# Performance work log

Measured on AMD Instinct MI355X. Metric: run time of the kernel, lower is better.

The kernel has to match this reference:

```python
import jax, jax.numpy as jnp
import numpy as np


def setup_inputs() -> dict:
    key = jax.random.key(0)
    k1, k2, k3 = jax.random.split(key, 3)
    N, C, H, W, K = 4, 128, 40, 30, 64
    return {
        "x": jax.random.normal(k1, (N, C, H, W), dtype=jnp.float32),
        "conv_w": jax.random.normal(k2, (K, C), dtype=jnp.float32) * 0.1,  # 1x1 conv weight [K,C,1,1] squeezed
        "centroids": jax.random.uniform(k3, (K, C), dtype=jnp.float32),
        "patch_size": 5,
        "stride": 1,
    }


def reference(x, conv_w, centroids, patch_size, stride):
    N, C, H, W = x.shape
    K = centroids.shape[0]
    # descriptor-wise L2 normalization (torch F.normalize semantics, eps=1e-12)
    norm = jnp.sqrt(jnp.sum(x * x, axis=1, keepdims=True))
    xn = x / jnp.maximum(norm, 1e-12)
    # 1x1 conv (no bias) + softmax over clusters -> soft assignment [N,K,H,W]
    logits = jnp.einsum('nchw,kc->nkhw', xn, conv_w)
    sa = jax.nn.softmax(logits, axis=1)
    # residuals [N,K,C,H,W]: (x - c_k) * a_k, then flatten K,C
    res = (xn[:, None, :, :, :] - centroids[None, :, :, None, None]) * sa[:, :, None, :, :]
    res = res.reshape(N, K * C, H, W)
    # 2D integral image with top-left zero padding -> [N,KC,H+1,W+1]
    I = jnp.cumsum(jnp.cumsum(res, axis=-1), axis=-2)
    I = jnp.pad(I, ((0, 0), (0, 0), (1, 0), (1, 0)))
    # box-filter via integral-image differencing (equivalent to the grouped
    # dilated 2x2 conv with weights [[+1,-1],[-1,+1]], stride=s, dilation=p)
    p, s = int(patch_size), int(stride)
    out = (I[:, :, p::s, p::s] - I[:, :, p::s, :-p:s]
           - I[:, :, :-p:s, p::s] + I[:, :, :-p:s, :-p:s])
    return out / (p * p)
```

## Files before the change

kernel.cpp:

```cpp
#include <hip/hip_runtime.h>

#define C_ 128
#define K_ 64
#define H_ 40
#define W_ 30
#define N_ 4
#define HW_ 1200
#define P_ 5
#define OH_ 36
#define OW_ 26
#define OHW_ 936

template<int CTRL>
__device__ __forceinline__ float dpp0f(float v) {
  return __int_as_float(__builtin_amdgcn_update_dpp(
      0, __float_as_int(v), CTRL, 0xF, 0xF, true));
}
__device__ __forceinline__ float swz_x16(float v) {
  return __int_as_float(__builtin_amdgcn_ds_swizzle(__float_as_int(v), 0x401F));
}

__global__ __launch_bounds__(256) void k1_prep(
    const float* __restrict__ x, const float* __restrict__ cw,
    float* __restrict__ xn, float* __restrict__ sa)
{
  __shared__ float xs[C_][32];
  __shared__ float wt[C_][K_];
  __shared__ float part[8][32];
  __shared__ float ls[K_][32];
  __shared__ float rnorm_s[32];
  __shared__ float rsum_s[32];

  const int tid  = threadIdx.x;
  const int pix0 = blockIdx.x << 5;

  for (int e = tid; e < C_*K_; e += 256) {
    const int c = e >> 6, kk = e & 63;
    wt[c][kk] = cw[kk*C_ + c];
  }
  for (int e = tid; e < C_*32; e += 256) {
    const int c = e >> 5, pl = e & 31;
    const int pix = pix0 + pl;
    const int n = pix / HW_, rem = pix - n*HW_;
    xs[c][pl] = x[(size_t)(n*C_ + c)*HW_ + rem];
  }
  __syncthreads();
  {
    const int pl = tid & 31, cq = tid >> 5;
    float s = 0.f;
    #pragma unroll
    for (int cc = 0; cc < 16; ++cc) {
      const float v = xs[cq*16 + cc][pl];
      s = fmaf(v, v, s);
    }
    part[cq][pl] = s;
  }
  __syncthreads();
  if (tid < 32) {
    float s = 0.f;
    #pragma unroll
    for (int qq = 0; qq < 8; ++qq) s += part[qq][tid];
    rnorm_s[tid] = 1.f / fmaxf(sqrtf(s), 1e-12f);
  }
  __syncthreads();
  {
    const int pl = tid & 31, kq = tid >> 5;
    float acc[8];
    #pragma unroll
    for (int qq = 0; qq < 8; ++qq) acc[qq] = 0.f;
    for (int c = 0; c < C_; ++c) {
      const float xv = xs[c][pl];
      const float4 w0 = *(const float4*)&wt[c][kq*8];
      const float4 w1 = *(const float4*)&wt[c][kq*8 + 4];
      acc[0] = fmaf(xv, w0.x, acc[0]);
      acc[1] = fmaf(xv, w0.y, acc[1]);
      acc[2] = fmaf(xv, w0.z, acc[2]);
      acc[3] = fmaf(xv, w0.w, acc[3]);
      acc[4] = fmaf(xv, w1.x, acc[4]);
      acc[5] = fmaf(xv, w1.y, acc[5]);
      acc[6] = fmaf(xv, w1.z, acc[6]);
      acc[7] = fmaf(xv, w1.w, acc[7]);
    }
    const float rn = rnorm_s[pl];
    #pragma unroll
    for (int qq = 0; qq < 8; ++qq) ls[kq*8 + qq][pl] = acc[qq] * rn;
  }
  __syncthreads();
  if (tid < 32) {
    const int pl = tid;
    float m = -1e30f;
    for (int kk = 0; kk < K_; ++kk) m = fmaxf(m, ls[kk][pl]);
    float s = 0.f;
    for (int kk = 0; kk < K_; ++kk) {
      const float e = expf(ls[kk][pl] - m);
      ls[kk][pl] = e;
      s += e;
    }
    rsum_s[pl] = 1.f / s;
  }
  __syncthreads();
  for (int e = tid; e < K_*32; e += 256) {
    const int kk = e >> 5, pl = e & 31;
    const int pix = pix0 + pl;
    const int n = pix / HW_, rem = pix - n*HW_;
    sa[(size_t)(n*K_ + kk)*HW_ + rem] = ls[kk][pl] * rsum_s[pl];
  }
  for (int e = tid; e < C_*32; e += 256) {
    const int c = e >> 5, pl = e & 31;
    const int pix = pix0 + pl;
    const int n = pix / HW_, rem = pix - n*HW_;
    xn[(size_t)(n*C_ + c)*HW_ + rem] = xs[c][pl] * rnorm_s[pl];
  }
}

__global__ __launch_bounds__(256, 6) void k2_box(
    const float* __restrict__ xn, const float* __restrict__ sa,
    const float* __restrict__ cent, float* __restrict__ out)
{
  const int tid = threadIdx.x;
  const int w   = tid & 31;
  const int wc  = (w < W_) ? w : (W_ - 1);
  const int c   = (blockIdx.x << 3) + (tid >> 5);
  const int k   = blockIdx.y;
  const int nh  = blockIdx.z;
  const int n   = nh >> 1;
  const int r0  = (nh & 1) * 18;

  const float cv = cent[k*C_ + c];
  const float* __restrict__ xp = xn + (size_t)(n*C_ + c)*HW_ + (size_t)r0*W_ + wc;
  const float* __restrict__ sp = sa + (size_t)(n*K_ + k)*HW_ + (size_t)r0*W_ + wc;

  float q[22];
  #pragma unroll
  for (int h = 0; h < 22; ++h) {
    q[h] = (xp[h*W_] - cv) * sp[h*W_];
  }

  float vq = q[0] + q[1] + q[2] + q[3] + q[4];
  float* __restrict__ op = out + (size_t)((n*K_ + k)*C_ + c)*OHW_
                               + (size_t)r0*OW_ + w;

  #pragma unroll
  for (int i = 0; i < 18; ++i) {
    const float sw = swz_x16(vq);
    float hs = vq;
    hs += dpp0f<0x101>(vq) + dpp0f<0x11F>(sw);
    hs += dpp0f<0x102>(vq) + dpp0f<0x11E>(sw);
    hs += dpp0f<0x103>(vq) + dpp0f<0x11D>(sw);
    hs += dpp0f<0x104>(vq) + dpp0f<0x11C>(sw);
    if (w < OW_) op[i*OW_] = hs * (1.f / (P_*P_));
    if (i < 17) vq += q[i + P_] - q[i];
  }
}

extern "C" void kernel_launch(void* const* d_in, const int* in_sizes, int n_in,
                              void* d_out, int out_size, void* d_ws, size_t ws_size,
                              hipStream_t stream) {
  const float* x  = (const float*)d_in[0];
  const float* cw = (const float*)d_in[1];
  const float* ce = (const float*)d_in[2];

  float* xn = (float*)d_ws;
  float* sa = xn + (size_t)N_*C_*HW_;
  float* out = (float*)d_out;

  k1_prep<<<dim3(150), dim3(256), 0, stream>>>(x, cw, xn, sa);
  k2_box<<<dim3(C_/8, K_, N_*2), dim3(256), 0, stream>>>(xn, sa, ce, out);
}
```

Before: 46.04 us.

## Split prep kernel into norm, logits, and softmax kernels

Replaces the single shared-memory prep kernel with three kernels: per-pixel L2 norm plus normalized output, a logits GEMV spread over 8 cluster groups per pixel block, and a softmax across 4 waves with a shared-memory reduction. The goal is more parallelism in the prep stage, which previously ran in only 150 blocks with serial single-wave softmax and transpose-staged weights. In exchange it adds two more kernel launches, a logits round trip through global memory, and reads x twice.

```diff
diff --git a/kernel.cpp b/kernel.cpp
--- a/kernel.cpp
+++ b/kernel.cpp
@@ -20,97 +20,112 @@
   return __int_as_float(__builtin_amdgcn_ds_swizzle(__float_as_int(v), 0x401F));
 }
 
-__global__ __launch_bounds__(256) void k1_prep(
+__global__ __launch_bounds__(64) void k1a_norm(
+    const float* __restrict__ x, float* __restrict__ xn,
+    float* __restrict__ rnorm)
+{
+  const int apix = (blockIdx.x << 6) + threadIdx.x;
+  const int n   = apix / HW_;
+  const int rem = apix - n*HW_;
+  const float* __restrict__ xp = x + (size_t)n*C_*HW_ + rem;
+
+  float s0 = 0.f, s1 = 0.f, s2 = 0.f, s3 = 0.f;
+  #pragma unroll 8
+  for (int c = 0; c < C_; c += 4) {
+    const float v0 = xp[(c+0)*HW_];
+    const float v1 = xp[(c+1)*HW_];
+    const float v2 = xp[(c+2)*HW_];
+    const float v3 = xp[(c+3)*HW_];
+    s0 = fmaf(v0, v0, s0); s1 = fmaf(v1, v1, s1);
+    s2 = fmaf(v2, v2, s2); s3 = fmaf(v3, v3, s3);
+  }
+  const float rn = 1.f / fmaxf(sqrtf((s0 + s1) + (s2 + s3)), 1e-12f);
+  rnorm[apix] = rn;
+
+  float* __restrict__ xo = xn + (size_t)n*C_*HW_ + rem;
+  #pragma unroll 8
+  for (int c = 0; c < C_; ++c) xo[c*HW_] = xp[c*HW_] * rn;
+}
+
+__global__ __launch_bounds__(64) void k1b_logits(
     const float* __restrict__ x, const float* __restrict__ cw,
-    float* __restrict__ xn, float* __restrict__ sa)
+    const float* __restrict__ rnorm, float* __restrict__ logits)
 {
-  __shared__ float xs[C_][32];
-  __shared__ float wt[C_][K_];
-  __shared__ float part[8][32];
-  __shared__ float ls[K_][32];
-  __shared__ float rnorm_s[32];
-  __shared__ float rsum_s[32];
+  const int apix = (blockIdx.x << 6) + threadIdx.x;
+  const int kq   = blockIdx.y;
+  const int n   = apix / HW_;
+  const int rem = apix - n*HW_;
+  const float* __restrict__ xp = x + (size_t)n*C_*HW_ + rem;
 
-  const int tid  = threadIdx.x;
-  const int pix0 = blockIdx.x << 5;
+  float acc[8];
+  #pragma unroll
+  for (int j = 0; j < 8; ++j) acc[j] = 0.f;
 
-  for (int e = tid; e < C_*K_; e += 256) {
-    const int c = e >> 6, kk = e & 63;
-    wt[c][kk] = cw[kk*C_ + c];
+  for (int c0 = 0; c0 < C_; c0 += 16) {
+    float xv[16];
+    #pragma unroll
+    for (int j = 0; j < 16; ++j) xv[j] = xp[(c0 + j)*HW_];
+    #pragma unroll
+    for (int kk = 0; kk < 8; ++kk) {
+      const float* __restrict__ wr = cw + (kq*8 + kk)*C_ + c0;
+      const float4 w0 = *(const float4*)(wr + 0);
+      const float4 w1 = *(const float4*)(wr + 4);
+      const float4 w2 = *(const float4*)(wr + 8);
+      const float4 w3 = *(const float4*)(wr + 12);
+      float a = acc[kk];
+      a = fmaf(w0.x, xv[0],  a); a = fmaf(w0.y, xv[1],  a);
+      a = fmaf(w0.z, xv[2],  a); a = fmaf(w0.w, xv[3],  a);
+      a = fmaf(w1.x, xv[4],  a); a = fmaf(w1.y, xv[5],  a);
+      a = fmaf(w1.z, xv[6],  a); a = fmaf(w1.w, xv[7],  a);
+      a = fmaf(w2.x, xv[8],  a); a = fmaf(w2.y, xv[9],  a);
+      a = fmaf(w2.z, xv[10], a); a = fmaf(w2.w, xv[11], a);
+      a = fmaf(w3.x, xv[12], a); a = fmaf(w3.y, xv[13], a);
+      a = fmaf(w3.z, xv[14], a); a = fmaf(w3.w, xv[15], a);
+      acc[kk] = a;
+    }
   }
-  for (int e = tid; e < C_*32; e += 256) {
-    const int c = e >> 5, pl = e & 31;
-    const int pix = pix0 + pl;
-    const int n = pix / HW_, rem = pix - n*HW_;
-    xs[c][pl] = x[(size_t)(n*C_ + c)*HW_ + rem];
-  }
+  const float rn = rnorm[apix];
+  float* __restrict__ lp = logits + (size_t)(n*K_ + kq*8)*HW_ + rem;
+  #pragma unroll
+  for (int kk = 0; kk < 8; ++kk) lp[kk*HW_] = acc[kk] * rn;
+}
+
+__global__ __launch_bounds__(256) void k1c_softmax(
+    const float* __restrict__ logits, float* __restrict__ sa)
+{
+  __shared__ float red[8][64];
+
+  const int lane = threadIdx.x & 63;
+  const int wv   = threadIdx.x >> 6;
+  const int apix = (blockIdx.x << 6) + lane;
+  const int n   = apix / HW_;
+  const int rem = apix - n*HW_;
+  const float* __restrict__ lp = logits + (size_t)(n*K_ + wv*16)*HW_ + rem;
+
+  float v[16];
+  #pragma unroll
+  for (int j = 0; j < 16; ++j) v[j] = lp[j*HW_];
+
+  float mx = v[0];
+  #pragma unroll
+  for (int j = 1; j < 16; ++j) mx = fmaxf(mx, v[j]);
+  red[wv][lane] = mx;
   __syncthreads();
-  {
-    const int pl = tid & 31, cq = tid >> 5;
-    float s = 0.f;
-    #pragma unroll
-    for (int cc = 0; cc < 16; ++cc) {
-      const float v = xs[cq*16 + cc][pl];
-      s = fmaf(v, v, s);
-    }
-    part[cq][pl] = s;
-  }
+  mx = fmaxf(fmaxf(red[0][lane], red[1][lane]),
+             fmaxf(red[2][lane], red[3][lane]));
+
+  float e[16];
+  float sum = 0.f;
+  #pragma unroll
+  for (int j = 0; j < 16; ++j) { e[j] = expf(v[j] - mx); sum += e[j]; }
+  red[4 + wv][lane] = sum;
   __syncthreads();
-  if (tid < 32) {
-    float s = 0.f;
-    #pragma unroll
-    for (int qq = 0; qq < 8; ++qq) s += part[qq][tid];
-    rnorm_s[tid] = 1.f / fmaxf(sqrtf(s), 1e-12f);
-  }
-  __syncthreads();
-  {
-    const int pl = tid & 31, kq = tid >> 5;
-    float acc[8];
-    #pragma unroll
-    for (int qq = 0; qq < 8; ++qq) acc[qq] = 0.f;
-    for (int c = 0; c < C_; ++c) {
-      const float xv = xs[c][pl];
-      const float4 w0 = *(const float4*)&wt[c][kq*8];
-      const float4 w1 = *(const float4*)&wt[c][kq*8 + 4];
-      acc[0] = fmaf(xv, w0.x, acc[0]);
-      acc[1] = fmaf(xv, w0.y, acc[1]);
-      acc[2] = fmaf(xv, w0.z, acc[2]);
-      acc[3] = fmaf(xv, w0.w, acc[3]);
-      acc[4] = fmaf(xv, w1.x, acc[4]);
-      acc[5] = fmaf(xv, w1.y, acc[5]);
-      acc[6] = fmaf(xv, w1.z, acc[6]);
-      acc[7] = fmaf(xv, w1.w, acc[7]);
-    }
-    const float rn = rnorm_s[pl];
-    #pragma unroll
-    for (int qq = 0; qq < 8; ++qq) ls[kq*8 + qq][pl] = acc[qq] * rn;
-  }
-  __syncthreads();
-  if (tid < 32) {
-    const int pl = tid;
-    float m = -1e30f;
-    for (int kk = 0; kk < K_; ++kk) m = fmaxf(m, ls[kk][pl]);
-    float s = 0.f;
-    for (int kk = 0; kk < K_; ++kk) {
-      const float e = expf(ls[kk][pl] - m);
-      ls[kk][pl] = e;
-      s += e;
-    }
-    rsum_s[pl] = 1.f / s;
-  }
-  __syncthreads();
-  for (int e = tid; e < K_*32; e += 256) {
-    const int kk = e >> 5, pl = e & 31;
-    const int pix = pix0 + pl;
-    const int n = pix / HW_, rem = pix - n*HW_;
-    sa[(size_t)(n*K_ + kk)*HW_ + rem] = ls[kk][pl] * rsum_s[pl];
-  }
-  for (int e = tid; e < C_*32; e += 256) {
-    const int c = e >> 5, pl = e & 31;
-    const int pix = pix0 + pl;
-    const int n = pix / HW_, rem = pix - n*HW_;
-    xn[(size_t)(n*C_ + c)*HW_ + rem] = xs[c][pl] * rnorm_s[pl];
-  }
+  const float rs = 1.f / (((red[4][lane] + red[5][lane]) +
+                           (red[6][lane] + red[7][lane])));
+
+  float* __restrict__ sp = sa + (size_t)(n*K_ + wv*16)*HW_ + rem;
+  #pragma unroll
+  for (int j = 0; j < 16; ++j) sp[j*HW_] = e[j] * rs;
 }
 
 __global__ __launch_bounds__(256, 6) void k2_box(
@@ -160,10 +175,14 @@
   const float* cw = (const float*)d_in[1];
   const float* ce = (const float*)d_in[2];
 
-  float* xn = (float*)d_ws;
-  float* sa = xn + (size_t)N_*C_*HW_;
+  float* xn     = (float*)d_ws;
+  float* sa     = xn + (size_t)N_*C_*HW_;
+  float* logits = sa + (size_t)N_*K_*HW_;
+  float* rnorm  = logits + (size_t)N_*K_*HW_;
   float* out = (float*)d_out;
 
-  k1_prep<<<dim3(150), dim3(256), 0, stream>>>(x, cw, xn, sa);
-  k2_box<<<dim3(C_/8, K_, N_*2), dim3(256), 0, stream>>>(xn, sa, ce, out);
+  k1a_norm   <<<dim3(75),     dim3(64),  0, stream>>>(x, xn, rnorm);
+  k1b_logits <<<dim3(75, 8),  dim3(64),  0, stream>>>(x, cw, rnorm, logits);
+  k1c_softmax<<<dim3(75),     dim3(256), 0, stream>>>(logits, sa);
+  k2_box     <<<dim3(C_/8, K_, N_*2), dim3(256), 0, stream>>>(xn, sa, ce, out);
 }
```

Measured after the change: 64.41 us. 39.9% more time.

## Restructure prep kernel: 16-pixel tiles, vectorized IO, parallel softmax reductions

Applied to the files above, without the earlier changes.

The prep kernel now handles 16 pixels per block, which doubles the grid to 300 blocks. It drops the transposed weight copy in shared memory and reads conv weights straight from global memory as float4. Loads and stores of x, xn and sa are vectorized, and the softmax max and sum are split across all threads through a partial-reduction array instead of 32 serial threads. This targets the serial tail and the low block count in the prep stage, but that stage is likely a small share of total time next to the box kernel, which writes a large output.

```diff
diff --git a/kernel.cpp b/kernel.cpp
--- a/kernel.cpp
+++ b/kernel.cpp
@@ -10,6 +10,7 @@
 #define OH_ 36
 #define OW_ 26
 #define OHW_ 936
+#define PIX_ 16
 
 template<int CTRL>
 __device__ __forceinline__ float dpp0f(float v) {
@@ -20,96 +21,144 @@
   return __int_as_float(__builtin_amdgcn_ds_swizzle(__float_as_int(v), 0x401F));
 }
 
-__global__ __launch_bounds__(256) void k1_prep(
+__global__ __launch_bounds__(256) void k1_fused(
     const float* __restrict__ x, const float* __restrict__ cw,
     float* __restrict__ xn, float* __restrict__ sa)
 {
-  __shared__ float xs[C_][32];
-  __shared__ float wt[C_][K_];
-  __shared__ float part[8][32];
-  __shared__ float ls[K_][32];
-  __shared__ float rnorm_s[32];
-  __shared__ float rsum_s[32];
-
-  const int tid  = threadIdx.x;
-  const int pix0 = blockIdx.x << 5;
-
-  for (int e = tid; e < C_*K_; e += 256) {
-    const int c = e >> 6, kk = e & 63;
-    wt[c][kk] = cw[kk*C_ + c];
-  }
-  for (int e = tid; e < C_*32; e += 256) {
-    const int c = e >> 5, pl = e & 31;
-    const int pix = pix0 + pl;
-    const int n = pix / HW_, rem = pix - n*HW_;
-    xs[c][pl] = x[(size_t)(n*C_ + c)*HW_ + rem];
-  }
-  __syncthreads();
-  {
-    const int pl = tid & 31, cq = tid >> 5;
+  __shared__ float xs[PIX_][132];
+  __shared__ float ls[K_][PIX_ + 2];
+  __shared__ float red[PIX_][20];
+  __shared__ float rnorm_s[PIX_];
+  __shared__ float rsum_s[PIX_];
+
+  const int tid = threadIdx.x;
+  const int bid = blockIdx.x;
+  const int n   = bid / 75;
+  const int rem = (bid - n*75) * PIX_;
+  const float* __restrict__ xb = x + (size_t)n*C_*HW_ + rem;
+
+  {
+    const int c  = tid >> 2;
+    const int p0 = (tid & 3) << 2;
+    const float4 v0 = *(const float4*)(xb + (size_t)c*HW_ + p0);
+    xs[p0+0][c] = v0.x; xs[p0+1][c] = v0.y;
+    xs[p0+2][c] = v0.z; xs[p0+3][c] = v0.w;
+    const int c2 = c + 64;
+    const float4 v1 = *(const float4*)(xb + (size_t)c2*HW_ + p0);
+    xs[p0+0][c2] = v1.x; xs[p0+1][c2] = v1.y;
+    xs[p0+2][c2] = v1.z; xs[p0+3][c2] = v1.w;
+  }
+  __syncthreads();
+
+  {
+    const int pix = tid & 15, cq = tid >> 4;
+    const float4 a = *(const float4*)&xs[pix][cq*8];
+    const float4 b = *(const float4*)&xs[pix][cq*8 + 4];
+    red[pix][cq] = (a.x*a.x + a.y*a.y) + (a.z*a.z + a.w*a.w)
+                 + (b.x*b.x + b.y*b.y) + (b.z*b.z + b.w*b.w);
+  }
+  __syncthreads();
+  if (tid < PIX_) {
     float s = 0.f;
     #pragma unroll
-    for (int cc = 0; cc < 16; ++cc) {
-      const float v = xs[cq*16 + cc][pl];
-      s = fmaf(v, v, s);
+    for (int j = 0; j < 16; ++j) s += red[tid][j];
+    rnorm_s[tid] = 1.f / fmaxf(sqrtf(s), 1e-12f);
+  }
+  __syncthreads();
+
+  {
+    const int pix = tid & 15, kq = tid >> 4;
+    const float* __restrict__ w0 = cw + (kq*4 + 0)*C_;
+    const float* __restrict__ w1 = cw + (kq*4 + 1)*C_;
+    const float* __restrict__ w2 = cw + (kq*4 + 2)*C_;
+    const float* __restrict__ w3 = cw + (kq*4 + 3)*C_;
+    float a0 = 0.f, a1 = 0.f, a2 = 0.f, a3 = 0.f;
+    #pragma unroll 8
+    for (int c0 = 0; c0 < C_; c0 += 4) {
+      const float4 xv = *(const float4*)&xs[pix][c0];
+      const float4 wa = *(const float4*)(w0 + c0);
+      const float4 wb = *(const float4*)(w1 + c0);
+      const float4 wc = *(const float4*)(w2 + c0);
+      const float4 wd = *(const float4*)(w3 + c0);
+      a0 = fmaf(wa.x, xv.x, a0); a0 = fmaf(wa.y, xv.y, a0);
+      a0 = fmaf(wa.z, xv.z, a0); a0 = fmaf(wa.w, xv.w, a0);
+      a1 = fmaf(wb.x, xv.x, a1); a1 = fmaf(wb.y, xv.y, a1);
+      a1 = fmaf(wb.z, xv.z, a1); a1 = fmaf(wb.w, xv.w, a1);
+      a2 = fmaf(wc.x, xv.x, a2); a2 = fmaf(wc.y, xv.y, a2);
+      a2 = fmaf(wc.z, xv.z, a2); a2 = fmaf(wc.w, xv.w, a2);
+      a3 = fmaf(wd.x, xv.x, a3); a3 = fmaf(wd.y, xv.y, a3);
+      a3 = fmaf(wd.z, xv.z, a3); a3 = fmaf(wd.w, xv.w, a3);
     }
-    part[cq][pl] = s;
-  }
-  __syncthreads();
-  if (tid < 32) {
+    const float rn = rnorm_s[pix];
+    ls[kq*4 + 0][pix] = a0 * rn;
+    ls[kq*4 + 1][pix] = a1 * rn;
+    ls[kq*4 + 2][pix] = a2 * rn;
+    ls[kq*4 + 3][pix] = a3 * rn;
+  }
+  {
+    const int c  = tid >> 2;
+    const int p0 = (tid & 3) << 2;
+    float4 o0, o1;
+    o0.x = xs[p0+0][c] * rnorm_s[p0+0];
+    o0.y = xs[p0+1][c] * rnorm_s[p0+1];
+    o0.z = xs[p0+2][c] * rnorm_s[p0+2];
+    o0.w = xs[p0+3][c] * rnorm_s[p0+3];
+    *(float4*)(xn + ((size_t)n*C_ + c)*HW_ + rem + p0) = o0;
+    const int c2 = c + 64;
+    o1.x = xs[p0+0][c2] * rnorm_s[p0+0];
+    o1.y = xs[p0+1][c2] * rnorm_s[p0+1];
+    o1.z = xs[p0+2][c2] * rnorm_s[p0+2];
+    o1.w = xs[p0+3][c2] * rnorm_s[p0+3];
+    *(float4*)(xn + ((size_t)n*C_ + c2)*HW_ + rem + p0) = o1;
+  }
+  __syncthreads();
+
+  {
+    const int pix = tid & 15, kq = tid >> 4;
+    const float v0 = ls[kq*4 + 0][pix];
+    const float v1 = ls[kq*4 + 1][pix];
+    const float v2 = ls[kq*4 + 2][pix];
+    const float v3 = ls[kq*4 + 3][pix];
+    red[pix][kq] = fmaxf(fmaxf(v0, v1), fmaxf(v2, v3));
+  }
+  __syncthreads();
+  if (tid < PIX_) {
+    float m = red[tid][0];
+    #pragma unroll
+    for (int j = 1; j < 16; ++j) m = fmaxf(m, red[tid][j]);
+    rnorm_s[tid] = m;
+  }
+  __syncthreads();
+  {
+    const int pix = tid & 15, kq = tid >> 4;
+    const float m = rnorm_s[pix];
+    const float e0 = expf(ls[kq*4 + 0][pix] - m);
+    const float e1 = expf(ls[kq*4 + 1][pix] - m);
+    const float e2 = expf(ls[kq*4 + 2][pix] - m);
+    const float e3 = expf(ls[kq*4 + 3][pix] - m);
+    ls[kq*4 + 0][pix] = e0;
+    ls[kq*4 + 1][pix] = e1;
+    ls[kq*4 + 2][pix] = e2;
+    ls[kq*4 + 3][pix] = e3;
+    red[pix][kq] = (e0 + e1) + (e2 + e3);
+  }
+  __syncthreads();
+  if (tid < PIX_) {
     float s = 0.f;
     #pragma unroll
-    for (int qq = 0; qq < 8; ++qq) s += part[qq][tid];
-    rnorm_s[tid] = 1.f / fmaxf(sqrtf(s), 1e-12f);
-  }
-  __syncthreads();
-  {
-    const int pl = tid & 31, kq = tid >> 5;
-    float acc[8];
-    #pragma unroll
-    for (int qq = 0; qq < 8; ++qq) acc[qq] = 0.f;
-    for (int c = 0; c < C_; ++c) {
-      const float xv = xs[c][pl];
-      const float4 w0 = *(const float4*)&wt[c][kq*8];
-      const float4 w1 = *(const float4*)&wt[c][kq*8 + 4];
-      acc[0] = fmaf(xv, w0.x, acc[0]);
-      acc[1] = fmaf(xv, w0.y, acc[1]);
-      acc[2] = fmaf(xv, w0.z, acc[2]);
-      acc[3] = fmaf(xv, w0.w, acc[3]);
-      acc[4] = fmaf(xv, w1.x, acc[4]);
-      acc[5] = fmaf(xv, w1.y, acc[5]);
-      acc[6] = fmaf(xv, w1.z, acc[6]);
-      acc[7] = fmaf(xv, w1.w, acc[7]);
-    }
-    const float rn = rnorm_s[pl];
-    #pragma unroll
-    for (int qq = 0; qq < 8; ++qq) ls[kq*8 + qq][pl] = acc[qq] * rn;
-  }
-  __syncthreads();
-  if (tid < 32) {
-    const int pl = tid;
-    float m = -1e30f;
-    for (int kk = 0; kk < K_; ++kk) m = fmaxf(m, ls[kk][pl]);
-    float s = 0.f;
-    for (int kk = 0; kk < K_; ++kk) {
-      const float e = expf(ls[kk][pl] - m);
-      ls[kk][pl] = e;
-      s += e;
-    }
-    rsum_s[pl] = 1.f / s;
-  }
-  __syncthreads();
-  for (int e = tid; e < K_*32; e += 256) {
-    const int kk = e >> 5, pl = e & 31;
-    const int pix = pix0 + pl;
-    const int n = pix / HW_, rem = pix - n*HW_;
-    sa[(size_t)(n*K_ + kk)*HW_ + rem] = ls[kk][pl] * rsum_s[pl];
-  }
-  for (int e = tid; e < C_*32; e += 256) {
-    const int c = e >> 5, pl = e & 31;
-    const int pix = pix0 + pl;
-    const int n = pix / HW_, rem = pix - n*HW_;
-    xn[(size_t)(n*C_ + c)*HW_ + rem] = xs[c][pl] * rnorm_s[pl];
+    for (int j = 0; j < 16; ++j) s += red[tid][j];
+    rsum_s[tid] = 1.f / s;
+  }
+  __syncthreads();
+  {
+    const int k  = tid >> 2;
+    const int p0 = (tid & 3) << 2;
+    float4 o;
+    o.x = ls[k][p0+0] * rsum_s[p0+0];
+    o.y = ls[k][p0+1] * rsum_s[p0+1];
+    o.z = ls[k][p0+2] * rsum_s[p0+2];
+    o.w = ls[k][p0+3] * rsum_s[p0+3];
+    *(float4*)(sa + ((size_t)n*K_ + k)*HW_ + rem + p0) = o;
   }
 }
 
@@ -164,6 +213,6 @@
   float* sa = xn + (size_t)N_*C_*HW_;
   float* out = (float*)d_out;
 
-  k1_prep<<<dim3(150), dim3(256), 0, stream>>>(x, cw, xn, sa);
-  k2_box<<<dim3(C_/8, K_, N_*2), dim3(256), 0, stream>>>(xn, sa, ce, out);
-}
+  k1_fused<<<dim3(300), dim3(256), 0, stream>>>(x, cw, xn, sa);
+  k2_box  <<<dim3(C_/8, K_, N_*2), dim3(256), 0, stream>>>(xn, sa, ce, out);
+}
```

Result: faster. 42.99 us (-6.6%).
